# Kernel tuning notes

Measured on AMD Instinct MI355X. Metric: run time of the kernel, lower is better.

Reference implementation:

```python
import jax, jax.numpy as jnp
import numpy as np

NUM_ITERATIONS = 5
EPSILON_0 = 1.0
EPS = 1e-20


def setup_inputs() -> dict:
    key = jax.random.key(0)
    k1, k2 = jax.random.split(key)
    B, NIN, NOUT = 8192, 3072, 512
    x = jax.random.uniform(k1, (B, NIN), dtype=jnp.float32)
    w = jax.random.uniform(k2, (NOUT, NIN), dtype=jnp.float32)
    # weights setter normalizes rows to sum to 1
    w = w / w.sum(axis=1, keepdims=True)
    h_initial = jnp.full((NOUT,), 1.0 / NOUT, dtype=jnp.float32)
    return {"x": x, "weights": w, "h_initial": h_initial}


def reference(x, weights, h_initial):
    # x: [B, NIN], weights: [NOUT, NIN], h_initial: [NOUT]
    x = x / (x.sum(axis=1, keepdims=True) + EPS)  # input normalization in forward()
    B = x.shape[0]
    h = jnp.broadcast_to(h_initial[None, :], (B, h_initial.shape[0]))

    def step(h, _):
        # Original: h_w = h[:,:,None]*W[None]; h_w /= h_w.sum(1,keepdim)+eps;
        #           h_w = (h_w * x[:,None,:]).sum(-1)
        # Equivalent without materializing [B, NOUT, NIN]:
        denom = h @ weights                       # [B, NIN] = sum_n h_bn W_nk
        h_w = h * ((x / (denom + EPS)) @ weights.T)  # [B, NOUT]
        h_new = h + EPSILON_0 * h_w               # epsilon_0 > 0 branch
        h_new = h_new / (h_new.sum(axis=1, keepdims=True) + EPS)
        return h_new, None

    h, _ = jax.lax.scan(step, h, None, length=NUM_ITERATIONS)
    return h
```

## Files before the change

### kernel.cpp

```cpp
#include <hip/hip_runtime.h>


#define NIN 3072
#define NOUT 512

using f32x4 = __attribute__((ext_vector_type(4))) float;
using i32x8 = __attribute__((ext_vector_type(8))) int;

union frag32 { i32x8 v; uint4 q[2]; };

#define MFMA128(A, B, C) \
    __builtin_amdgcn_mfma_scale_f32_16x16x128_f8f6f4( \
        (A), (B), (C), 0, 0, 0, (int)0x7f7f7f7f, 0, (int)0x7f7f7f7f)
#define MFMA128_F6(A, B, C) \
    __builtin_amdgcn_mfma_scale_f32_16x16x128_f8f6f4( \
        (A), (B), (C), 0, 2, 0, (int)0x7f7f7f7f, 0, (int)0x7f7f7f7f)

__device__ __forceinline__ unsigned enc_fp6(float p) {
    if (p < 1.9375f) {
        int q = (int)rintf(p * 8.0f);
        return (unsigned)q;
    }
    if (p < 3.875f) {
        int m = (int)rintf((p - 2.0f) * 4.0f);
        return (m > 7) ? 24u : (16u + (unsigned)m);
    }
    int m = (int)rintf((p - 4.0f) * 2.0f);
    if (m > 7) m = 7;
    return 24u + (unsigned)m;
}

__device__ __forceinline__ void load6(frag32& f, const unsigned char* p) {
    const uint2* q = reinterpret_cast<const uint2*>(p);
    uint2 a = q[0], b = q[1], c = q[2];
    f.v = (i32x8){(int)a.x, (int)a.y, (int)b.x, (int)b.y, (int)c.x, (int)c.y, 0, 0};
}

#define LDS_BARRIER() do {                                   \
    asm volatile("s_waitcnt lgkmcnt(0)" ::: "memory");       \
    __builtin_amdgcn_s_barrier();                            \
    asm volatile("" ::: "memory");                           \
} while (0)

__global__ void prep_w(const float* __restrict__ W,
                       const float* __restrict__ h_init,
                       unsigned char* __restrict__ W1,
                       unsigned char* __restrict__ W2,
                       float* __restrict__ d0part) {
    __shared__ float tile[64][132];
    const int bb = blockIdx.x;
    const int t  = threadIdx.x;
    const int s  = bb >> 3, nc = bb & 7;
    const int n0 = nc * 64, k0 = s * 128;

    {
        int r8 = t >> 5, c4 = (t & 31) << 2;
        #pragma unroll
        for (int pass = 0; pass < 8; ++pass) {
            int r = pass * 8 + r8;
            float4 v = *reinterpret_cast<const float4*>(
                &W[(size_t)(n0 + r) * NIN + k0 + c4]);
            tile[r][c4] = v.x; tile[r][c4 + 1] = v.y;
            tile[r][c4 + 2] = v.z; tile[r][c4 + 3] = v.w;
        }
    }
    __syncthreads();

    {
        int ntl = t >> 6, l = t & 63, lo = l & 15, hi = l >> 4;
        int n_loc = ntl * 16 + lo;
        int kk = hi * 32;
        unsigned int words[8];
        #pragma unroll
        for (int q = 0; q < 8; ++q) {
            float v0 = tile[n_loc][kk + q * 4 + 0] * 4096.0f;
            float v1 = tile[n_loc][kk + q * 4 + 1] * 4096.0f;
            float v2 = tile[n_loc][kk + q * 4 + 2] * 4096.0f;
            float v3 = tile[n_loc][kk + q * 4 + 3] * 4096.0f;
            int pk = __builtin_amdgcn_cvt_pk_fp8_f32(v0, v1, 0, false);
            pk     = __builtin_amdgcn_cvt_pk_fp8_f32(v2, v3, pk, true);
            words[q] = (unsigned int)pk;
        }
        uint4* dst = reinterpret_cast<uint4*>(
            W2 + ((size_t)((s * 32 + nc * 4 + ntl) * 64 + l)) * 32);
        dst[0] = *reinterpret_cast<uint4*>(&words[0]);
        dst[1] = *reinterpret_cast<uint4*>(&words[4]);
    }

    {
        int w8 = t >> 5, r5 = t & 31, l15 = r5 & 15, hs = r5 >> 4;
        int hi = ((nc & 1) << 1) + hs;
        int l  = hi * 16 + l15;
        int c  = nc >> 1;
        int kout_loc = w8 * 16 + l15;
        unsigned int dw[6] = {0, 0, 0, 0, 0, 0};
        #pragma unroll
        for (int j = 0; j < 32; ++j) {
            float p = tile[hs * 32 + j][kout_loc] * 8192.0f;
            unsigned c6 = enc_fp6(p);
            int bit = 6 * j, di = bit >> 5, off = bit & 31;
            dw[di] |= c6 << off;
            if (off > 26) dw[di + 1] |= c6 >> (32 - off);
        }
        uint2* d2 = reinterpret_cast<uint2*>(
            W1 + ((size_t)(((s * 8 + w8) * 4 + c) * 64 + l)) * 24);
        d2[0] = make_uint2(dw[0], dw[1]);
        d2[1] = make_uint2(dw[2], dw[3]);
        d2[2] = make_uint2(dw[4], dw[5]);
    }

    if (t < 128) {
        float ssum = 0.f;
        #pragma unroll 8
        for (int r = 0; r < 64; ++r)
            ssum += h_init[n0 + r] * tile[r][t];
        d0part[(size_t)(k0 + t) * 8 + nc] = ssum;
    }
}

__global__ __launch_bounds__(512, 1) void nnmf_main(
    const float* __restrict__ x,
    const unsigned char* __restrict__ W1,
    const unsigned char* __restrict__ W2,
    const float* __restrict__ d0part,
    const float* __restrict__ h_init,
    float* __restrict__ out)
{
    __shared__ unsigned char  h8_lds[32 * 528];
    __shared__ float          h32_lds[32 * 516];
    __shared__ float          x_lds[32 * 132];
    __shared__ unsigned char  r8_lds[32 * 144];
    __shared__ float red[8][32];
    __shared__ float rfac_lds[32];

    const int tid = threadIdx.x;
    const int w  = tid >> 6;
    const int l  = tid & 63;
    const int lo = l & 15;
    const int hi = l >> 4;
    const int b0 = blockIdx.x * 32;

    for (int idx = tid; idx < 32 * 512; idx += 512) {
        int r = idx >> 9, c = idx & 511;
        h32_lds[r * 516 + c] = h_init[c];
    }

    const int xrow = tid >> 4, xcc = tid & 15;
    const uint4* xg = reinterpret_cast<const uint4*>(x + (size_t)(b0 + xrow) * NIN);
    float* xdstA = &x_lds[xrow * 132 + xcc * 4];
    float* xdstB = &x_lds[xrow * 132 + 64 + xcc * 4];

    const unsigned char* w1base = W1 + ((size_t)(w * 4) * 64 + l) * 24;
    const unsigned char* w2base = W2 + (size_t)w * 8192 + (size_t)l * 32;

    *reinterpret_cast<uint4*>(xdstA) = xg[xcc];
    *reinterpret_cast<uint4*>(xdstB) = xg[16 + xcc];
    uint4 xnA = xg[32 + xcc], xnB = xg[48 + xcc];
    frag32 w1buf[4];
    __syncthreads();

    const float DSCL2 = 3.0517578125e-05f;
    f32x4 tacc[2][4];
    float xs0[4], xs1[4];
    #pragma unroll
    for (int i = 0; i < 4; ++i) { xs0[i] = 0.f; xs1[i] = 0.f; }

    for (int it = 0; it < 5; ++it) {
        #pragma unroll
        for (int m = 0; m < 2; ++m)
            #pragma unroll
            for (int nt = 0; nt < 4; ++nt)
                tacc[m][nt] = (f32x4){0.f, 0.f, 0.f, 0.f};

        for (int s = 0; s < 24; ++s) {
            const int sn  = (s + 1 == 24) ? 0 : s + 1;
            const int sn2 = (s + 2 >= 24) ? (s + 2 - 24) : s + 2;

            frag32 w2v[4];
            {
                const unsigned char* w2p = w2base + (size_t)s * 65536;
                #pragma unroll
                for (int nt = 0; nt < 4; ++nt) {
                    const uint4* p = reinterpret_cast<const uint4*>(w2p + nt * 2048);
                    w2v[nt].q[0] = p[0];
                    w2v[nt].q[1] = p[1];
                }
            }

            f32x4 d0 = {0,0,0,0}, d1 = {0,0,0,0};
            float dv = 0.f;
            if (it == 0) {
                const float4* dp4 = reinterpret_cast<const float4*>(
                    d0part + (size_t)(s * 128 + w * 16 + lo) * 8);
                float4 a = dp4[0], b = dp4[1];
                float sm = 1e-20f + a.x + a.y + a.z + a.w + b.x + b.y + b.z + b.w;
                dv = 0.015625f / sm;
            } else {
                #pragma unroll
                for (int c = 0; c < 4; ++c) {
                    frag32 ha0, ha1;
                    const uint4* p0 = reinterpret_cast<const uint4*>(
                        &h8_lds[lo * 528 + c * 128 + hi * 32]);
                    const uint4* p1 = reinterpret_cast<const uint4*>(
                        &h8_lds[(16 + lo) * 528 + c * 128 + hi * 32]);
                    ha0.q[0] = p0[0]; ha0.q[1] = p0[1];
                    ha1.q[0] = p1[0]; ha1.q[1] = p1[1];
                    d0 = MFMA128_F6(ha0.v, w1buf[c].v, d0);
                    d1 = MFMA128_F6(ha1.v, w1buf[c].v, d1);
                }
            }

            #pragma unroll
            for (int i = 0; i < 4; ++i) {
                int row0 = hi * 4 + i;
                float x0 = x_lds[row0 * 132 + w * 16 + lo];
                float x1 = x_lds[(16 + row0) * 132 + w * 16 + lo];
                float r0, r1;
                if (it == 0) {
                    r0 = x0 * dv; r1 = x1 * dv;
                    xs0[i] += x0; xs1[i] += x1;
                } else {
                    r0 = x0 * __builtin_amdgcn_rcpf(fmaf(d0[i], DSCL2, 1e-20f));
                    r1 = x1 * __builtin_amdgcn_rcpf(fmaf(d1[i], DSCL2, 1e-20f));
                }
                int c0 = __builtin_amdgcn_cvt_pk_fp8_f32(r0, r0, 0, false);
                int c1 = __builtin_amdgcn_cvt_pk_fp8_f32(r1, r1, 0, false);
                r8_lds[row0 * 144 + w * 16 + lo] = (unsigned char)(c0 & 0xff);
                r8_lds[(16 + row0) * 144 + w * 16 + lo] = (unsigned char)(c1 & 0xff);
            }
            LDS_BARRIER();

            frag32 ra0, ra1;
            {
                const uint4* p0 = reinterpret_cast<const uint4*>(&r8_lds[lo * 144 + hi * 32]);
                const uint4* p1 = reinterpret_cast<const uint4*>(&r8_lds[(16 + lo) * 144 + hi * 32]);
                ra0.q[0] = p0[0]; ra0.q[1] = p0[1];
                ra1.q[0] = p1[0]; ra1.q[1] = p1[1];
            }
            #pragma unroll
            for (int nt = 0; nt < 2; ++nt) {
                tacc[0][nt] = MFMA128(ra0.v, w2v[nt].v, tacc[0][nt]);
                tacc[1][nt] = MFMA128(ra1.v, w2v[nt].v, tacc[1][nt]);
            }

            if (it > 0 || s == 23) {
                const unsigned char* w1p = w1base + (size_t)sn * 49152;
                #pragma unroll
                for (int c = 0; c < 4; ++c)
                    load6(w1buf[c], w1p + c * 1536);
            }

            #pragma unroll
            for (int nt = 2; nt < 4; ++nt) {
                tacc[0][nt] = MFMA128(ra0.v, w2v[nt].v, tacc[0][nt]);
                tacc[1][nt] = MFMA128(ra1.v, w2v[nt].v, tacc[1][nt]);
            }

            *reinterpret_cast<uint4*>(xdstA) = xnA;
            *reinterpret_cast<uint4*>(xdstB) = xnB;
            xnA = xg[(size_t)sn2 * 32 + xcc];
            xnB = xg[(size_t)sn2 * 32 + 16 + xcc];
            LDS_BARRIER();
        }

        if (it == 0) {
            #pragma unroll
            for (int mask = 1; mask < 16; mask <<= 1)
                #pragma unroll
                for (int i = 0; i < 4; ++i) {
                    xs0[i] += __shfl_xor(xs0[i], mask, 64);
                    xs1[i] += __shfl_xor(xs1[i], mask, 64);
                }
            if (lo == 0) {
                #pragma unroll
                for (int i = 0; i < 4; ++i) {
                    red[w][hi * 4 + i]      = xs0[i];
                    red[w][16 + hi * 4 + i] = xs1[i];
                }
            }
            __syncthreads();
            if (tid < 32) {
                float sme = 1e-20f;
                #pragma unroll
                for (int ww = 0; ww < 8; ++ww) sme += red[ww][tid];
                rfac_lds[tid] = 0.015625f / sme;
            }
            __syncthreads();
        }

        float hv_[2][4][4];
        float p[2][4];
        float rf[2][4];
        #pragma unroll
        for (int m = 0; m < 2; ++m)
            #pragma unroll
            for (int i = 0; i < 4; ++i) {
                p[m][i] = 0.f;
                rf[m][i] = rfac_lds[m * 16 + hi * 4 + i];
            }

        #pragma unroll
        for (int m = 0; m < 2; ++m)
            #pragma unroll
            for (int nt = 0; nt < 4; ++nt)
                #pragma unroll
                for (int i = 0; i < 4; ++i) {
                    int row = m * 16 + hi * 4 + i;
                    int col = w * 64 + nt * 16 + lo;
                    float hv = h32_lds[row * 516 + col];
                    float v = hv * fmaf(tacc[m][nt][i], rf[m][i], 1.0f);
                    hv_[m][nt][i] = v;
                    p[m][i] += v;
                }
        #pragma unroll
        for (int mask = 1; mask < 16; mask <<= 1)
            #pragma unroll
            for (int m = 0; m < 2; ++m)
                #pragma unroll
                for (int i = 0; i < 4; ++i)
                    p[m][i] += __shfl_xor(p[m][i], mask, 64);
        if (lo == 0) {
            #pragma unroll
            for (int m = 0; m < 2; ++m)
                #pragma unroll
                for (int i = 0; i < 4; ++i)
                    red[w][m * 16 + hi * 4 + i] = p[m][i];
        }
        __syncthreads();
        float inv[2][4];
        #pragma unroll
        for (int m = 0; m < 2; ++m)
            #pragma unroll
            for (int i = 0; i < 4; ++i) {
                int row = m * 16 + hi * 4 + i;
                float S = 0.f;
                #pragma unroll
                for (int ww = 0; ww < 8; ++ww) S += red[ww][row];
                inv[m][i] = 1.f / (S + 1e-20f);
            }

        if (it < 4) {
            #pragma unroll
            for (int m = 0; m < 2; ++m)
                #pragma unroll
                for (int nt = 0; nt < 4; ++nt)
                    #pragma unroll
                    for (int i = 0; i < 4; ++i) {
                        int row = m * 16 + hi * 4 + i;
                        int col = w * 64 + nt * 16 + lo;
                        float hv = hv_[m][nt][i] * inv[m][i];
                        h32_lds[row * 516 + col] = hv;
                        int c = __builtin_amdgcn_cvt_pk_fp8_f32(hv * 256.0f, hv * 256.0f, 0, false);
                        h8_lds[row * 528 + col] = (unsigned char)(c & 0xff);
                    }
            __syncthreads();
        } else {
            #pragma unroll
            for (int m = 0; m < 2; ++m)
                #pragma unroll
                for (int nt = 0; nt < 4; ++nt)
                    #pragma unroll
                    for (int i = 0; i < 4; ++i) {
                        int row = m * 16 + hi * 4 + i;
                        int col = w * 64 + nt * 16 + lo;
                        out[(size_t)(b0 + row) * 512 + col] = hv_[m][nt][i] * inv[m][i];
                    }
        }
    }
}

extern "C" void kernel_launch(void* const* d_in, const int* in_sizes, int n_in,
                              void* d_out, int out_size, void* d_ws, size_t ws_size,
                              hipStream_t stream) {
    const float* x   = (const float*)d_in[0];
    const float* wgt = (const float*)d_in[1];
    const float* h0  = (const float*)d_in[2];
    float* out = (float*)d_out;

    unsigned char* W1 = (unsigned char*)d_ws;
    unsigned char* W2 = (unsigned char*)((char*)d_ws + 1179648);
    float* d0part     = (float*)((char*)d_ws + 2752512);

    prep_w<<<192, 256, 0, stream>>>(wgt, h0, W1, W2, d0part);
    nnmf_main<<<256, 512, 0, stream>>>(x, W1, W2, d0part, h0, out);
}
```

Baseline: 407.0 us.

## Stash x as bf16 copy in workspace during first iteration to halve reread traffic

```diff
diff --git a/kernel.cpp b/kernel.cpp
--- a/kernel.cpp
+++ b/kernel.cpp
@@ -15,6 +15,21 @@
 #define MFMA128_F6(A, B, C) \
     __builtin_amdgcn_mfma_scale_f32_16x16x128_f8f6f4( \
         (A), (B), (C), 0, 2, 0, (int)0x7f7f7f7f, 0, (int)0x7f7f7f7f)
+
+__device__ __forceinline__ unsigned short f2bf(float f) {
+    unsigned int u = __builtin_bit_cast(unsigned int, f);
+    return (unsigned short)((u + 0x7fffu + ((u >> 16) & 1u)) >> 16);
+}
+__device__ __forceinline__ float bf2f(unsigned short s) {
+    unsigned int u = ((unsigned int)s) << 16;
+    return __builtin_bit_cast(float, u);
+}
+__device__ __forceinline__ ushort4 f2bf4(uint4 u) {
+    float4 f = __builtin_bit_cast(float4, u);
+    ushort4 o;
+    o.x = f2bf(f.x); o.y = f2bf(f.y); o.z = f2bf(f.z); o.w = f2bf(f.w);
+    return o;
+}
 
 __device__ __forceinline__ unsigned enc_fp6(float p) {
     if (p < 1.9375f) {
@@ -120,6 +135,7 @@
 
 __global__ __launch_bounds__(512, 1) void nnmf_main(
     const float* __restrict__ x,
+    unsigned short* __restrict__ X2,
     const unsigned char* __restrict__ W1,
     const unsigned char* __restrict__ W2,
     const float* __restrict__ d0part,
@@ -128,10 +144,13 @@
 {
     __shared__ unsigned char  h8_lds[32 * 528];
     __shared__ float          h32_lds[32 * 516];
-    __shared__ float          x_lds[32 * 132];
+    __shared__ __align__(16) unsigned char xbuf[32 * 132 * 4];
     __shared__ unsigned char  r8_lds[32 * 144];
     __shared__ float red[8][32];
     __shared__ float rfac_lds[32];
+
+    float* x32 = reinterpret_cast<float*>(xbuf);
+    unsigned short* x16 = reinterpret_cast<unsigned short*>(xbuf);
 
     const int tid = threadIdx.x;
     const int w  = tid >> 6;
@@ -146,16 +165,25 @@
     }
 
     const int xrow = tid >> 4, xcc = tid & 15;
-    const uint4* xg = reinterpret_cast<const uint4*>(x + (size_t)(b0 + xrow) * NIN);
-    float* xdstA = &x_lds[xrow * 132 + xcc * 4];
-    float* xdstB = &x_lds[xrow * 132 + 64 + xcc * 4];
+    const uint4* xg32 = reinterpret_cast<const uint4*>(x + (size_t)(b0 + xrow) * NIN);
+    const uint4* xg16 = reinterpret_cast<const uint4*>(X2 + (size_t)(b0 + xrow) * NIN + xcc * 8);
+    unsigned short* x2w = X2 + (size_t)(b0 + xrow) * NIN;
+    float* x32dstA = &x32[xrow * 132 + xcc * 4];
+    float* x32dstB = &x32[xrow * 132 + 64 + xcc * 4];
+    unsigned short* x16dst = &x16[xrow * 136 + xcc * 8];
 
     const unsigned char* w1base = W1 + ((size_t)(w * 4) * 64 + l) * 24;
     const unsigned char* w2base = W2 + (size_t)w * 8192 + (size_t)l * 32;
 
-    *reinterpret_cast<uint4*>(xdstA) = xg[xcc];
-    *reinterpret_cast<uint4*>(xdstB) = xg[16 + xcc];
-    uint4 xnA = xg[32 + xcc], xnB = xg[48 + xcc];
+    {
+        uint4 a0 = xg32[xcc], a1 = xg32[16 + xcc];
+        *reinterpret_cast<uint4*>(x32dstA) = a0;
+        *reinterpret_cast<uint4*>(x32dstB) = a1;
+        *reinterpret_cast<ushort4*>(x2w + xcc * 4) = f2bf4(a0);
+        *reinterpret_cast<ushort4*>(x2w + 64 + xcc * 4) = f2bf4(a1);
+    }
+    uint4 xnA = xg32[32 + xcc], xnB = xg32[48 + xcc];
+    uint4 xn16;
     frag32 w1buf[4];
     __syncthreads();
 
@@ -210,23 +238,32 @@
                 }
             }
 
-            #pragma unroll
-            for (int i = 0; i < 4; ++i) {
-                int row0 = hi * 4 + i;
-                float x0 = x_lds[row0 * 132 + w * 16 + lo];
-                float x1 = x_lds[(16 + row0) * 132 + w * 16 + lo];
-                float r0, r1;
-                if (it == 0) {
-                    r0 = x0 * dv; r1 = x1 * dv;
+            if (it == 0) {
+                #pragma unroll
+                for (int i = 0; i < 4; ++i) {
+                    int row0 = hi * 4 + i;
+                    float x0 = x32[row0 * 132 + w * 16 + lo];
+                    float x1 = x32[(16 + row0) * 132 + w * 16 + lo];
                     xs0[i] += x0; xs1[i] += x1;
-                } else {
-                    r0 = x0 * __builtin_amdgcn_rcpf(fmaf(d0[i], DSCL2, 1e-20f));
-                    r1 = x1 * __builtin_amdgcn_rcpf(fmaf(d1[i], DSCL2, 1e-20f));
-                }
-                int c0 = __builtin_amdgcn_cvt_pk_fp8_f32(r0, r0, 0, false);
-                int c1 = __builtin_amdgcn_cvt_pk_fp8_f32(r1, r1, 0, false);
-                r8_lds[row0 * 144 + w * 16 + lo] = (unsigned char)(c0 & 0xff);
-                r8_lds[(16 + row0) * 144 + w * 16 + lo] = (unsigned char)(c1 & 0xff);
+                    float r0 = x0 * dv, r1 = x1 * dv;
+                    int c0 = __builtin_amdgcn_cvt_pk_fp8_f32(r0, r0, 0, false);
+                    int c1 = __builtin_amdgcn_cvt_pk_fp8_f32(r1, r1, 0, false);
+                    r8_lds[row0 * 144 + w * 16 + lo] = (unsigned char)(c0 & 0xff);
+                    r8_lds[(16 + row0) * 144 + w * 16 + lo] = (unsigned char)(c1 & 0xff);
+                }
+            } else {
+                #pragma unroll
+                for (int i = 0; i < 4; ++i) {
+                    int row0 = hi * 4 + i;
+                    float x0 = bf2f(x16[row0 * 136 + w * 16 + lo]);
+                    float x1 = bf2f(x16[(16 + row0) * 136 + w * 16 + lo]);
+                    float r0 = x0 * __builtin_amdgcn_rcpf(fmaf(d0[i], DSCL2, 1e-20f));
+                    float r1 = x1 * __builtin_amdgcn_rcpf(fmaf(d1[i], DSCL2, 1e-20f));
+                    int c0 = __builtin_amdgcn_cvt_pk_fp8_f32(r0, r0, 0, false);
+                    int c1 = __builtin_amdgcn_cvt_pk_fp8_f32(r1, r1, 0, false);
+                    r8_lds[row0 * 144 + w * 16 + lo] = (unsigned char)(c0 & 0xff);
+                    r8_lds[(16 + row0) * 144 + w * 16 + lo] = (unsigned char)(c1 & 0xff);
+                }
             }
             LDS_BARRIER();
 
@@ -256,10 +293,21 @@
                 tacc[1][nt] = MFMA128(ra1.v, w2v[nt].v, tacc[1][nt]);
             }
 
-            *reinterpret_cast<uint4*>(xdstA) = xnA;
-            *reinterpret_cast<uint4*>(xdstB) = xnB;
-            xnA = xg[(size_t)sn2 * 32 + xcc];
-            xnB = xg[(size_t)sn2 * 32 + 16 + xcc];
+            if (it == 0) {
+                if (s < 23) {
+                    *reinterpret_cast<uint4*>(x32dstA) = xnA;
+                    *reinterpret_cast<uint4*>(x32dstB) = xnB;
+                    *reinterpret_cast<ushort4*>(x2w + (s + 1) * 128 + xcc * 4) = f2bf4(xnA);
+                    *reinterpret_cast<ushort4*>(x2w + (s + 1) * 128 + 64 + xcc * 4) = f2bf4(xnB);
+                    if (s < 22) {
+                        xnA = xg32[(s + 2) * 32 + xcc];
+                        xnB = xg32[(s + 2) * 32 + 16 + xcc];
+                    }
+                }
+            } else {
+                *reinterpret_cast<uint4*>(x16dst) = xn16;
+                xn16 = xg16[(size_t)sn2 * 16];
+            }
             LDS_BARRIER();
         }
 
@@ -286,6 +334,10 @@
                 rfac_lds[tid] = 0.015625f / sme;
             }
             __syncthreads();
+            asm volatile("s_waitcnt vmcnt(0)" ::: "memory");
+            uint4 v0 = xg16[0];
+            *reinterpret_cast<uint4*>(x16dst) = v0;
+            xn16 = xg16[16];
         }
 
         float hv_[2][4][4];
@@ -377,10 +429,11 @@
     const float* h0  = (const float*)d_in[2];
     float* out = (float*)d_out;
 
-    unsigned char* W1 = (unsigned char*)d_ws;
-    unsigned char* W2 = (unsigned char*)((char*)d_ws + 1179648);
-    float* d0part     = (float*)((char*)d_ws + 2752512);
+    unsigned short* X2 = (unsigned short*)d_ws;
+    unsigned char*  W1 = (unsigned char*)((char*)d_ws + 50331648);
+    unsigned char*  W2 = (unsigned char*)((char*)d_ws + 51511296);
+    float* d0part      = (float*)((char*)d_ws + 53084160);
 
     prep_w<<<192, 256, 0, stream>>>(wgt, h0, W1, W2, d0part);
-    nnmf_main<<<256, 512, 0, stream>>>(x, W1, W2, d0part, h0, out);
-}
+    nnmf_main<<<256, 512, 0, stream>>>(x, X2, W1, W2, d0part, h0, out);
+}
```

Result: slower. 419.9 us (+3.2%).
